# Kernel optimization log

Hardware: AMD Instinct MI355X
Metric: run time of the kernel (lower is better)

The kernel has to match this reference:

```python
import jax, jax.numpy as jnp
import numpy as np

GAMMA = 0.25      # commitment loss weight (bn.gamma)
STRIDE = 8        # LCCombine upsample stride (embedding rate -> wav rate)
FILTER = 9        # LCCombine local filter size

B, Q, N = 4, 64, 4096
K = 512
C = 256
T = (N - 1) * STRIDE + FILTER - 1  # 32768


def setup_inputs() -> dict:
    key = jax.random.key(0)
    k1, k2, k3, k4, k5 = jax.random.split(key, 5)
    quant_pred = jax.random.normal(k1, (B, C, T), dtype=jnp.float32)
    target_wav = jax.random.randint(k2, (B, T), 0, C, dtype=jnp.int32)
    ze = jax.random.normal(k3, (B, Q, N), dtype=jnp.float32)
    emb = jax.random.normal(k4, (K, Q), dtype=jnp.float32)
    combine_w = jax.random.uniform(k5, (FILTER,), dtype=jnp.float32) / FILTER
    return {"quant_pred": quant_pred, "target_wav": target_wav,
            "ze": ze, "emb": emb, "combine_w": combine_w}


def _lc_combine(x, w):
    # x: (B, 1, N) per-embedding-timestep loss; transposed local conv -> (B, 1, (N-1)*S+F)
    kern = w.reshape(1, 1, FILTER)  # OIH
    return jax.lax.conv_transpose(x, kern, strides=(STRIDE,), padding='VALID',
                                  dimension_numbers=('NCH', 'OIH', 'NCH'))


def reference(quant_pred, target_wav, ze, emb, combine_w):
    sg = jax.lax.stop_gradient
    # pairwise squared L2 distances without the (B,K,Q,N) broadcast:
    # d[b,k,n] = ||ze[b,:,n]||^2 + ||emb[k]||^2 - 2 <ze[b,:,n], emb[k]>
    ze2 = jnp.sum(ze * ze, axis=1)                      # (B, N)
    emb2 = jnp.sum(emb * emb, axis=1)                   # (K,)
    cross = jnp.einsum('bqn,kq->bkn', ze, emb)          # (B, K, N)
    dist = ze2[:, None, :] + emb2[None, :, None] - 2.0 * cross
    ind = jnp.argmin(dist, axis=1)                      # (B, N)
    emb_sel = emb[ind]                                  # (B, N, Q)
    ze_t = jnp.transpose(ze, (0, 2, 1))                 # (B, N, Q)
    # codebook loss: grad to emb only (StopGrad on ze)
    l2_loss_embeds = jnp.sum((sg(ze_t) - emb_sel) ** 2, axis=-1)        # (B, N)
    # commitment loss: grad to ze only (bn.l2norm_min uses sg(emb))
    com_loss_embeds = GAMMA * jnp.sum((ze_t - sg(emb_sel)) ** 2, axis=-1)
    # local-conv combine to wav rate, drop last timestep
    l2_loss_ts = _lc_combine(l2_loss_embeds[:, None, :], combine_w)[..., :-1]   # (B,1,T)
    com_loss_ts = _lc_combine(com_loss_embeds[:, None, :], combine_w)[..., :-1]
    # reconstruction: gathered log-softmax
    log_pred = jax.nn.log_softmax(quant_pred, axis=1)   # (B, C, T)
    log_pred_target = jnp.take_along_axis(log_pred, target_wav[:, None, :], axis=1)  # (B,1,T)
    total_loss_ts = -log_pred_target + l2_loss_ts + com_loss_ts
    return jnp.mean(total_loss_ts)
```

## Files before the change

kernel.cpp:

```cpp
#include <hip/hip_runtime.h>
#include <hip/hip_bf16.h>

static constexpr int Qq = 64, Nn = 4096, Kk = 512, Cc = 256, Tt = 32768;
static constexpr float kLog2e = 1.4426950408889634f;
static constexpr float kLn2 = 0.6931471805599453f;
static constexpr float kInvCount = 1.0f / 131072.0f;

typedef short bf16x8 __attribute__((ext_vector_type(8)));
typedef float f32x4 __attribute__((ext_vector_type(4)));

static __device__ __forceinline__ ushort bf16bits(float f) {
  __hip_bfloat16 h = __float2bfloat16(f);
  return *(ushort*)&h;
}

static __device__ __forceinline__ bf16x8 cvt8(const float* __restrict__ p) {
  float4 a0 = *(const float4*)p;
  float4 a1 = *(const float4*)(p + 4);
  bf16x8 r;
  r[0] = (short)bf16bits(a0.x); r[1] = (short)bf16bits(a0.y);
  r[2] = (short)bf16bits(a0.z); r[3] = (short)bf16bits(a0.w);
  r[4] = (short)bf16bits(a1.x); r[5] = (short)bf16bits(a1.y);
  r[6] = (short)bf16bits(a1.z); r[7] = (short)bf16bits(a1.w);
  return r;
}

__global__ __launch_bounds__(256) void fused_kernel(const float* __restrict__ qp,
                                                    const int* __restrict__ tgt,
                                                    const float* __restrict__ ze,
                                                    const float* __restrict__ emb,
                                                    const float* __restrict__ cw,
                                                    float* __restrict__ part) {
  __shared__ __align__(16) float smem[3456];
  const int tid = threadIdx.x;
  const int bid = blockIdx.x;

  if (bid % 3 == 0) {
    ushort* zs = (ushort*)smem;
    float* e2s = smem + 2304;
    unsigned long long* red = (unsigned long long*)(smem + 2816);

    const int vb = bid / 3;
    const int b = vb >> 6;
    const int n0 = (vb & 63) << 6;
    const float* zebase = ze + (size_t)b * Qq * Nn + n0;

    {
      const int nc = tid & 15;
      const int q0 = tid >> 4;
#pragma unroll
      for (int it = 0; it < 4; ++it) {
        int q = q0 + 16 * it;
        float4 v = *(const float4*)(zebase + (size_t)q * Nn + 4 * nc);
        zs[(4 * nc + 0) * 72 + q] = bf16bits(v.x);
        zs[(4 * nc + 1) * 72 + q] = bf16bits(v.y);
        zs[(4 * nc + 2) * 72 + q] = bf16bits(v.z);
        zs[(4 * nc + 3) * 72 + q] = bf16bits(v.w);
      }
    }
    for (int k = tid; k < Kk; k += 256) {
      const float4* row = (const float4*)(emb + (size_t)k * Qq);
      float a = 0.f;
#pragma unroll
      for (int i = 0; i < 16; ++i) {
        float4 f = row[i];
        a += f.x * f.x + f.y * f.y + f.z * f.z + f.w * f.w;
      }
      e2s[k] = a;
    }
    __syncthreads();

    const int w = tid >> 6, lane = tid & 63;
    const int lc = lane & 15;
    const int lg = lane >> 4;

    bf16x8 bfr[4][2];
#pragma unroll
    for (int ct = 0; ct < 4; ++ct)
#pragma unroll
      for (int ks = 0; ks < 2; ++ks)
        bfr[ct][ks] = *(const bf16x8*)&zs[(ct * 16 + lc) * 72 + ks * 32 + lg * 8];

    unsigned long long pk[4] = {~0ull, ~0ull, ~0ull, ~0ull};
#pragma unroll 2
    for (int mt = 0; mt < 8; ++mt) {
      const int arow = w * 128 + mt * 16 + lc;
      const float* ap = emb + (size_t)arow * Qq;
      f32x4 acc[4] = {{0.f, 0.f, 0.f, 0.f}, {0.f, 0.f, 0.f, 0.f},
                      {0.f, 0.f, 0.f, 0.f}, {0.f, 0.f, 0.f, 0.f}};
#pragma unroll
      for (int ks = 0; ks < 2; ++ks) {
        bf16x8 af = cvt8(ap + ks * 32 + lg * 8);
#pragma unroll
        for (int ct = 0; ct < 4; ++ct)
          acc[ct] = __builtin_amdgcn_mfma_f32_16x16x32_bf16(af, bfr[ct][ks],
                                                            acc[ct], 0, 0, 0);
      }
      const int kbase = w * 128 + mt * 16 + lg * 4;
#pragma unroll
      for (int r = 0; r < 4; ++r) {
        int k = kbase + r;
        float e2v = e2s[k];
#pragma unroll
        for (int ct = 0; ct < 4; ++ct) {
          float sc = e2v - 2.0f * acc[ct][r];
          unsigned u = __float_as_uint(sc);
          u = (u & 0x80000000u) ? ~u : (u | 0x80000000u);
          unsigned long long p = ((unsigned long long)u << 32) | (unsigned)k;
          pk[ct] = (p < pk[ct]) ? p : pk[ct];
        }
      }
    }

#pragma unroll
    for (int ct = 0; ct < 4; ++ct) {
      unsigned long long o = __shfl_xor(pk[ct], 16);
      pk[ct] = (o < pk[ct]) ? o : pk[ct];
      o = __shfl_xor(pk[ct], 32);
      pk[ct] = (o < pk[ct]) ? o : pk[ct];
    }
    if (lane < 16) {
#pragma unroll
      for (int ct = 0; ct < 4; ++ct) red[w * 64 + ct * 16 + lane] = pk[ct];
    }
    __syncthreads();

    if (tid < 64) {
      unsigned long long mn = red[tid];
#pragma unroll
      for (int ww = 1; ww < 4; ++ww) {
        unsigned long long v = red[ww * 64 + tid];
        mn = (v < mn) ? v : mn;
      }
      int kb = (int)(unsigned)(mn & 0xffffffffull);

      const float* zc = zebase + tid;
      const float* er = emb + (size_t)kb * Qq;
      float l2 = 0.f;
#pragma unroll
      for (int q = 0; q < 64; ++q) {
        float d = zc[(size_t)q * Nn] - er[q];
        l2 += d * d;
      }
      float wacc = 0.f;
#pragma unroll
      for (int i = 0; i < 9; ++i) wacc += cw[i];
      if (n0 + tid == Nn - 1) wacc -= cw[0];
      float val = 1.25f * l2 * wacc;
#pragma unroll
      for (int off = 32; off > 0; off >>= 1) val += __shfl_down(val, off);
      if (tid == 0) part[512 + vb] = val;
    }
  } else {
    const int rb = bid - bid / 3 - 1;
    const int col = rb * 256 + tid;
    const int b = col >> 15;
    const int t = col & (Tt - 1);
    const int tg = tgt[col];
    const float* base = qp + (size_t)b * Cc * Tt + t;

    float s0 = 0.f, s1 = 0.f, s2 = 0.f, s3 = 0.f, V = 0.f;
#pragma unroll 1
    for (int c0 = 0; c0 < Cc; c0 += 32) {
      float v[32];
#pragma unroll
      for (int i = 0; i < 32; ++i) v[i] = base[(size_t)(c0 + i) * Tt];
#pragma unroll
      for (int i = 0; i < 32; ++i) {
        float e = __builtin_amdgcn_exp2f(v[i] * kLog2e);
        if ((i & 3) == 0) s0 += e;
        else if ((i & 3) == 1) s1 += e;
        else if ((i & 3) == 2) s2 += e;
        else s3 += e;
        V = (c0 + i == tg) ? v[i] : V;
      }
    }
    float S = (s0 + s1) + (s2 + s3);
    float contrib = kLn2 * __builtin_amdgcn_logf(S) - V;

#pragma unroll
    for (int off = 32; off > 0; off >>= 1) contrib += __shfl_down(contrib, off);
    float* wsum = smem + 3328;
    if ((tid & 63) == 0) wsum[tid >> 6] = contrib;
    __syncthreads();
    if (tid == 0) part[rb] = (wsum[0] + wsum[1]) + (wsum[2] + wsum[3]);
  }
}

__global__ __launch_bounds__(256) void final_kernel(const float* __restrict__ part,
                                                    float* __restrict__ out) {
  const int tid = threadIdx.x;
  float s = part[tid] + part[tid + 256] + part[tid + 512];
#pragma unroll
  for (int off = 32; off > 0; off >>= 1) s += __shfl_down(s, off);
  __shared__ float ws[4];
  if ((tid & 63) == 0) ws[tid >> 6] = s;
  __syncthreads();
  if (tid == 0) out[0] = ((ws[0] + ws[1]) + (ws[2] + ws[3])) * kInvCount;
}

extern "C" void kernel_launch(void* const* d_in, const int* in_sizes, int n_in,
                              void* d_out, int out_size, void* d_ws, size_t ws_size,
                              hipStream_t stream) {
  const float* qp  = (const float*)d_in[0];
  const int*   tgt = (const int*)d_in[1];
  const float* ze  = (const float*)d_in[2];
  const float* emb = (const float*)d_in[3];
  const float* cw  = (const float*)d_in[4];
  float* out = (float*)d_out;
  float* part = (float*)d_ws;

  fused_kernel<<<dim3(768), dim3(256), 0, stream>>>(qp, tgt, ze, emb, cw, part);
  final_kernel<<<dim3(1), dim3(256), 0, stream>>>(part, out);
}
```

Measured before the change: 31.17 us.

## Split log-softmax channels across waves with float4 column loads and LDS reduction

The log-softmax blocks now have each wave handle 64 of the 256 channels, with each lane loading float4 across 4 adjacent time columns instead of one scalar column per thread over all channels. Partial exp-sums and gathered target logits are combined across the four waves through shared memory. The goal is wider 16-byte loads, fewer serial iterations per thread and more independent accumulation chains. The cost is an extra LDS round trip and barrier, plus more live registers for the four-column state.

```diff
diff --git a/kernel.cpp b/kernel.cpp
--- a/kernel.cpp
+++ b/kernel.cpp
@@ -153,34 +153,48 @@
     }
   } else {
     const int rb = bid - bid / 3 - 1;
-    const int col = rb * 256 + tid;
-    const int b = col >> 15;
-    const int t = col & (Tt - 1);
-    const int tg = tgt[col];
-    const float* base = qp + (size_t)b * Cc * Tt + t;
-
-    float s0 = 0.f, s1 = 0.f, s2 = 0.f, s3 = 0.f, V = 0.f;
+    const int col0 = rb * 256;
+    const int b = col0 >> 15;
+    const int t0 = col0 & (Tt - 1);
+    const int l = tid & 63, w = tid >> 6;
+    const int c0base = w * 64;
+    const float* base = qp + (size_t)b * Cc * Tt + t0 + 4 * l;
+    const int4 tg4 = *(const int4*)(tgt + col0 + 4 * l);
+
+    float s0 = 0.f, s1 = 0.f, s2 = 0.f, s3 = 0.f;
+    float V0 = 0.f, V1 = 0.f, V2 = 0.f, V3 = 0.f;
 #pragma unroll 1
-    for (int c0 = 0; c0 < Cc; c0 += 32) {
-      float v[32];
-#pragma unroll
-      for (int i = 0; i < 32; ++i) v[i] = base[(size_t)(c0 + i) * Tt];
-#pragma unroll
-      for (int i = 0; i < 32; ++i) {
-        float e = __builtin_amdgcn_exp2f(v[i] * kLog2e);
-        if ((i & 3) == 0) s0 += e;
-        else if ((i & 3) == 1) s1 += e;
-        else if ((i & 3) == 2) s2 += e;
-        else s3 += e;
-        V = (c0 + i == tg) ? v[i] : V;
-      }
-    }
-    float S = (s0 + s1) + (s2 + s3);
+    for (int cc = 0; cc < 64; cc += 8) {
+      float4 v[8];
+#pragma unroll
+      for (int i = 0; i < 8; ++i)
+        v[i] = *(const float4*)(base + (size_t)(c0base + cc + i) * Tt);
+#pragma unroll
+      for (int i = 0; i < 8; ++i) {
+        int c = c0base + cc + i;
+        s0 += __builtin_amdgcn_exp2f(v[i].x * kLog2e);
+        s1 += __builtin_amdgcn_exp2f(v[i].y * kLog2e);
+        s2 += __builtin_amdgcn_exp2f(v[i].z * kLog2e);
+        s3 += __builtin_amdgcn_exp2f(v[i].w * kLog2e);
+        V0 = (c == tg4.x) ? v[i].x : V0;
+        V1 = (c == tg4.y) ? v[i].y : V1;
+        V2 = (c == tg4.z) ? v[i].z : V2;
+        V3 = (c == tg4.w) ? v[i].w : V3;
+      }
+    }
+    float* ss = smem;
+    float* vv = smem + 1024;
+    ((float4*)(ss + w * 256))[l] = make_float4(s0, s1, s2, s3);
+    ((float4*)(vv + w * 256))[l] = make_float4(V0, V1, V2, V3);
+    __syncthreads();
+
+    float S = (ss[tid] + ss[256 + tid]) + (ss[512 + tid] + ss[768 + tid]);
+    float V = (vv[tid] + vv[256 + tid]) + (vv[512 + tid] + vv[768 + tid]);
     float contrib = kLn2 * __builtin_amdgcn_logf(S) - V;
 
 #pragma unroll
     for (int off = 32; off > 0; off >>= 1) contrib += __shfl_down(contrib, off);
-    float* wsum = smem + 3328;
+    float* wsum = smem + 2048;
     if ((tid & 63) == 0) wsum[tid >> 6] = contrib;
     __syncthreads();
     if (tid == 0) part[rb] = (wsum[0] + wsum[1]) + (wsum[2] + wsum[3]);
```

Measured after the change: 35.27 us. 1.13x slower.
